# Optimization experiments

Measured on AMD Instinct MI355X. Metric: run time of the kernel, lower is better.

Reference implementation:

```python
import jax, jax.numpy as jnp
import numpy as np

DIM = 512; HEADS = 8; DH = 64; CHUNK = 64; DHID = DH * 4; MAX_LR = 1.0; EPS = 1e-6


def rmsnorm(x, w):
    return x * jax.lax.rsqrt(jnp.mean(x * x, axis=-1, keepdims=True) + EPS) * w


def mem_forward(params, x):
    # MemoryMLP(depth=2, expansion=4) wrapped in ResidualNorm
    nw, w0, w1 = params
    h = rmsnorm(x, nw)
    y = jax.nn.gelu(h @ w0) @ w1
    return y + x


def chunk_loss(params, k, lr, v):
    pred = mem_forward(params, k)            # (CHUNK, DH)
    loss = jnp.mean((pred - v) ** 2, axis=-1)  # per-token mse, (CHUNK,)
    return (loss * lr).sum(), loss


def assoc_scan(gates, inputs, prev=None):
    # h_t = g_t * h_{t-1} + x_t along axis=1 (chunks)
    def combine(a, b):
        g1, x1 = a; g2, x2 = b
        return g1 * g2, x2 + g2 * x1
    G, X = jax.lax.associative_scan(combine, (gates, inputs), axis=1)
    if prev is None:
        return X
    return X + G * prev[:, None]


def setup_inputs() -> dict:
    key = jax.random.key(0)
    ks = jax.random.split(key, 8)
    B, N = 2, 4096
    s = 0.02
    return {
        'seq': jax.random.normal(ks[0], (B, N, DIM), jnp.float32),
        'store_norm_w': jnp.ones((DIM,), jnp.float32),
        'Wk': jax.random.normal(ks[1], (DIM, HEADS * DH), jnp.float32) * s,
        'Wv': jax.random.normal(ks[2], (DIM, HEADS * DH), jnp.float32) * s,
        'Wstep': jax.random.normal(ks[3], (DIM, HEADS), jnp.float32) * s,
        'bstep': jnp.zeros((HEADS,), jnp.float32),
        'Wmom': jax.random.normal(ks[4], (DIM, HEADS), jnp.float32) * s,
        'bmom': jnp.zeros((HEADS,), jnp.float32),
        'Wdec': jax.random.normal(ks[5], (DIM, HEADS), jnp.float32) * s,
        'bdec': jnp.zeros((HEADS,), jnp.float32),
        'mem_norm_w': jnp.ones((HEADS, DH), jnp.float32),
        'mem_w0': jax.random.normal(ks[6], (HEADS, DH, DHID), jnp.float32) * s,
        'mem_w1': jax.random.normal(ks[7], (HEADS, DHID, DH), jnp.float32) * s,
    }


def reference(seq, store_norm_w, Wk, Wv, Wstep, bstep, Wmom, bmom, Wdec, bdec, mem_norm_w, mem_w0, mem_w1):
    B, N, _ = seq.shape
    nc = N // CHUNK
    bh = B * HEADS
    x = rmsnorm(seq, store_norm_w)                        # store pre-norm, (B,N,D)
    # per-token adaptive lr: 'b n h -> (b h) n', sigmoid * max_lr
    lr = jax.nn.sigmoid(x @ Wstep + bstep) * MAX_LR       # (B,N,H)
    lr = lr.transpose(0, 2, 1).reshape(bh, nc, CHUNK)
    # chunk-pooled rep (AveragePool) -> momentum / decay gates per chunk
    pooled = x.reshape(B, nc, CHUNK, DIM).mean(axis=2)    # (B,nc,D)
    mom = jax.nn.sigmoid(pooled @ Wmom + bmom).transpose(0, 2, 1).reshape(bh, nc, 1)
    decay = jax.nn.sigmoid(pooled @ Wdec + bdec).transpose(0, 2, 1).reshape(bh, nc, 1)

    def split(t):  # (B,N,H*DH) -> (bh, nc, CHUNK, DH)
        return t.reshape(B, N, HEADS, DH).transpose(0, 2, 1, 3).reshape(bh, nc, CHUNK, DH)
    k = split(x @ Wk)
    v = split(x @ Wv)

    # initial fast weights per (b h) stream: repeat 'h ... -> (b h) ...'
    params0 = (jnp.tile(mem_norm_w, (B, 1)),
               jnp.tile(mem_w0, (B, 1, 1)),
               jnp.tile(mem_w1, (B, 1, 1)))

    # per-chunk per-stream grads via vmap(grad) (all chunks share the initial weights)
    grad_fn = jax.grad(chunk_loss, has_aux=True)
    per_chunk = jax.vmap(grad_fn, in_axes=(None, 0, 0, 0))
    per_bh = jax.vmap(per_chunk, in_axes=(0, 0, 0, 0))
    grads, _ = per_bh(params0, k, lr, v)                  # tuple of (bh, nc, *shape)

    finals = []
    for g, w0 in zip(grads, params0):
        surprise = -g
        extra = (1,) * (g.ndim - 2)
        m = mom.reshape(bh, nc, *extra)
        d = decay.reshape(bh, nc, *extra)
        update = assoc_scan(m, surprise)                  # momentum scan, zero init
        wts = assoc_scan(1.0 - d, update, prev=w0)        # decay recurrence from init weights
        finals.append(wts[:, -1].reshape(bh, -1))
    return jnp.concatenate(finals, axis=-1)              # (bh, DH + DH*DHID + DHID*DH)
```

## Files before the change

### kernel.cpp

```cpp
#include <hip/hip_runtime.h>
#include <math.h>

typedef __attribute__((ext_vector_type(8)))  __bf16 bf16x8;
typedef __attribute__((ext_vector_type(4)))  float  f32x4;
typedef __attribute__((ext_vector_type(4)))  unsigned short ushort4v;
typedef __attribute__((ext_vector_type(8)))  unsigned short ushort8v;

#define MFMA16(acc, a, b) acc = __builtin_amdgcn_mfma_f32_16x16x32_bf16((a),(b),(acc),0,0,0)

__device__ inline unsigned short f2b(float f) {
    union { float f; unsigned int u; } v; v.f = f;
    unsigned int r = v.u + 0x7FFFu + ((v.u >> 16) & 1u);
    return (unsigned short)(r >> 16);
}
__device__ inline float b2f(unsigned short h) {
    union { unsigned int u; float f; } v; v.u = ((unsigned int)h) << 16;
    return v.f;
}
__device__ inline float tanh_fast(float z) {
    float e = __expf(2.0f * z);
    return 1.0f - 2.0f / (e + 1.0f);
}
__device__ inline float gelu_g(float x) {
    const float c0 = 0.7978845608028654f, c1 = 0.044715f;
    float z = c0 * x * (1.0f + c1 * x * x);
    return 0.5f * x * (1.0f + tanh_fast(z));
}
__device__ inline void gelu_both(float x, float& g, float& gp) {
    const float c0 = 0.7978845608028654f, c1 = 0.044715f;
    float x2 = x * x;
    float z  = c0 * x * (1.0f + c1 * x2);
    float t  = tanh_fast(z);
    g  = 0.5f * x * (1.0f + t);
    float dz = c0 * (1.0f + 3.0f * c1 * x2);
    gp = 0.5f * (1.0f + t) + 0.5f * x * (1.0f - t * t) * dz;
}
__device__ inline float sigmoidf(float x) { return 1.0f / (1.0f + __expf(-x)); }

__global__ __launch_bounds__(256) void k_wprep(
    const float* __restrict__ Wk, const float* __restrict__ Wv,
    const float* __restrict__ w0_g, const float* __restrict__ w1_g,
    const float* __restrict__ nw_g,
    unsigned short* __restrict__ WkvT, unsigned short* __restrict__ w0fT,
    unsigned short* __restrict__ w1T, unsigned short* __restrict__ w0N,
    unsigned short* __restrict__ w1N)
{
    const int bid = blockIdx.x, tid = threadIdx.x;
    __shared__ float tile[64][65];
    if (bid < 128) {
        int kt = bid >> 4, nt = bid & 15;
        const float* src = (nt < 8) ? Wk : Wv;
        int ncol0 = (nt & 7) * 64;
        for (int ii = 0; ii < 16; ++ii) {
            int idx = tid + ii * 256; int r = idx >> 6, cc = idx & 63;
            tile[r][cc] = src[(size_t)(kt * 64 + r) * 512 + ncol0 + cc];
        }
        __syncthreads();
        for (int ii = 0; ii < 16; ++ii) {
            int idx = tid + ii * 256; int r = idx >> 6, cc = idx & 63;
            WkvT[(size_t)(nt * 64 + r) * 512 + kt * 64 + cc] = f2b(tile[cc][r]);
        }
    } else if (bid < 160) {
        int q = bid - 128; int hh = q >> 2, it = q & 3;
        const float* w0h = w0_g + hh * 16384;
        for (int ii = 0; ii < 16; ++ii) {
            int idx = tid + ii * 256; int r = idx >> 6, cc = idx & 63;
            tile[r][cc] = w0h[r * 256 + it * 64 + cc];
        }
        __syncthreads();
        for (int ii = 0; ii < 16; ++ii) {
            int idx = tid + ii * 256; int r = idx >> 6, cc = idx & 63;
            w0fT[hh * 16384 + (it * 64 + r) * 64 + cc] = f2b(nw_g[hh * 64 + cc] * tile[cc][r]);
        }
    } else if (bid < 192) {
        int q = bid - 160; int hh = q >> 2, it = q & 3;
        const float* w1h = w1_g + hh * 16384;
        for (int ii = 0; ii < 16; ++ii) {
            int idx = tid + ii * 256; int r = idx >> 6, cc = idx & 63;
            tile[r][cc] = w1h[(it * 64 + r) * 64 + cc];
        }
        __syncthreads();
        for (int ii = 0; ii < 16; ++ii) {
            int idx = tid + ii * 256; int r = idx >> 6, cc = idx & 63;
            w1T[hh * 16384 + r * 256 + it * 64 + cc] = f2b(tile[cc][r]);
        }
    } else {
        int q = bid - 192;
        int gid = q * 2048 + tid * 8;
        const float* s; unsigned short* d;
        if (gid < 131072) { s = w0_g + gid; d = w0N + gid; }
        else              { s = w1_g + (gid - 131072); d = w1N + (gid - 131072); }
        #pragma unroll
        for (int jj = 0; jj < 8; ++jj) d[jj] = f2b(s[jj]);
    }
}

__global__ __launch_bounds__(256) void k_rms_lr(
    const float* __restrict__ seq, const float* __restrict__ wnorm,
    const float* __restrict__ Wstep, const float* __restrict__ bstep,
    unsigned short* __restrict__ xb, float* __restrict__ lrb)
{
    const int wid = threadIdx.x >> 6, lane = threadIdx.x & 63;
    const int t = blockIdx.x * 4 + wid;
    const float* row = seq + (size_t)t * 512 + lane * 8;
    float v[8];
    *(f32x4*)&v[0] = *(const f32x4*)row;
    *(f32x4*)&v[4] = *(const f32x4*)(row + 4);
    float ss = 0.f;
    #pragma unroll
    for (int j = 0; j < 8; ++j) ss += v[j] * v[j];
    #pragma unroll
    for (int o = 1; o < 64; o <<= 1) ss += __shfl_xor(ss, o);
    float rr = rsqrtf(ss * (1.0f / 512.0f) + 1e-6f);
    const float* wn = wnorm + lane * 8;
    ushort8v xs;
    float acc[8] = {0.f,0.f,0.f,0.f,0.f,0.f,0.f,0.f};
    #pragma unroll
    for (int j = 0; j < 8; ++j) {
        float xf = v[j] * rr * wn[j];
        xs[j] = f2b(xf);
        const float* wrow = Wstep + (size_t)(lane * 8 + j) * 8;
        #pragma unroll
        for (int h = 0; h < 8; ++h) acc[h] = fmaf(xf, wrow[h], acc[h]);
    }
    *(ushort8v*)(xb + (size_t)t * 512 + lane * 8) = xs;
    #pragma unroll
    for (int h = 0; h < 8; ++h) {
        #pragma unroll
        for (int o = 1; o < 64; o <<= 1) acc[h] += __shfl_xor(acc[h], o);
    }
    if (lane == 0) {
        #pragma unroll
        for (int h = 0; h < 8; ++h) lrb[(size_t)t * 8 + h] = sigmoidf(acc[h] + bstep[h]);
    }
}

__global__ __launch_bounds__(256) void k_pool(
    const unsigned short* __restrict__ xb, float* __restrict__ pooled)
{
    const int bc = blockIdx.x, tid = threadIdx.x;
    float p0 = 0.f, p1 = 0.f;
    for (int t = 0; t < 64; ++t) {
        const unsigned short* r = xb + (size_t)(bc * 64 + t) * 512;
        p0 += b2f(r[tid]); p1 += b2f(r[tid + 256]);
    }
    pooled[(size_t)bc * 512 + tid]       = p0 * (1.0f / 64.0f);
    pooled[(size_t)bc * 512 + tid + 256] = p1 * (1.0f / 64.0f);
}

__global__ __launch_bounds__(256) void k_proj(
    const unsigned short* __restrict__ xb, const unsigned short* __restrict__ WkvT,
    float* __restrict__ kb, unsigned short* __restrict__ vb)
{
    __shared__ __attribute__((aligned(16))) unsigned short As[128][72];
    __shared__ __attribute__((aligned(16))) unsigned short Bs[128][72];
    const int tid = threadIdx.x;
    const int bm = blockIdx.x >> 3, bn = blockIdx.x & 7;
    const int m0 = bm * 128, n0 = bn * 128;
    const int wid = tid >> 6, lane = tid & 63, lg = lane >> 4, lo = lane & 15;
    const int wm = wid >> 1, wn = wid & 1;
    f32x4 acc[4][4];
    #pragma unroll
    for (int i = 0; i < 4; ++i)
        #pragma unroll
        for (int j = 0; j < 4; ++j) acc[i][j] = (f32x4)0.f;

    for (int k0 = 0; k0 < 512; k0 += 64) {
        #pragma unroll
        for (int ii = 0; ii < 4; ++ii) {
            int e0 = tid * 32 + ii * 8;
            int r = e0 >> 6, c = e0 & 63;
            *(bf16x8*)&As[r][c] = *(const bf16x8*)(xb   + (size_t)(m0 + r) * 512 + k0 + c);
            *(bf16x8*)&Bs[r][c] = *(const bf16x8*)(WkvT + (size_t)(n0 + r) * 512 + k0 + c);
        }
        __syncthreads();
        #pragma unroll
        for (int ks = 0; ks < 2; ++ks) {
            bf16x8 aF[4], bF[4];
            #pragma unroll
            for (int mt = 0; mt < 4; ++mt) aF[mt] = *(const bf16x8*)&As[wm * 64 + mt * 16 + lo][ks * 32 + 8 * lg];
            #pragma unroll
            for (int nt = 0; nt < 4; ++nt) bF[nt] = *(const bf16x8*)&Bs[wn * 64 + nt * 16 + lo][ks * 32 + 8 * lg];
            #pragma unroll
            for (int mt = 0; mt < 4; ++mt)
                #pragma unroll
                for (int nt = 0; nt < 4; ++nt) MFMA16(acc[mt][nt], aF[mt], bF[nt]);
        }
        __syncthreads();
    }
    #pragma unroll
    for (int mt = 0; mt < 4; ++mt)
        #pragma unroll
        for (int nt = 0; nt < 4; ++nt)
            #pragma unroll
            for (int r = 0; r < 4; ++r) {
                int row = m0 + wm * 64 + mt * 16 + lg * 4 + r;
                int col = n0 + wn * 64 + nt * 16 + lo;
                float val = acc[mt][nt][r];
                if (col < 512) kb[(size_t)row * 512 + col] = val;
                else           vb[(size_t)row * 512 + col - 512] = f2b(val);
            }
}

__global__ __launch_bounds__(64) void k_gates(
    const float* __restrict__ pooled,
    const float* __restrict__ Wmom, const float* __restrict__ bmom,
    const float* __restrict__ Wdec, const float* __restrict__ bdec,
    float* __restrict__ momout, float* __restrict__ decout)
{
    const int bc = blockIdx.x;
    const int tid = threadIdx.x, h = tid & 7, d0 = tid >> 3;
    const float* pr = pooled + (size_t)bc * 512;
    float pm = 0.f, pd = 0.f;
    #pragma unroll 8
    for (int it = 0; it < 64; ++it) {
        int d = d0 + it * 8; float pv = pr[d];
        pm = fmaf(pv, Wmom[d * 8 + h], pm);
        pd = fmaf(pv, Wdec[d * 8 + h], pd);
    }
    #pragma unroll
    for (int o = 8; o < 64; o <<= 1) { pm += __shfl_xor(pm, o); pd += __shfl_xor(pd, o); }
    if (tid < 8) {
        momout[(size_t)bc * 8 + h] = sigmoidf(pm + bmom[h]);
        decout[(size_t)bc * 8 + h] = sigmoidf(pd + bdec[h]);
    }
}

__global__ void k_coeff(const float* __restrict__ mom, const float* __restrict__ dec,
                        float* __restrict__ coeff, float* __restrict__ Aout)
{
    int s = threadIdx.x;
    if (s >= 16) return;
    int b = s >> 3, h = s & 7;
    float P = 1.f, S = 1.f;
    coeff[s * 64 + 63] = 1.f;
    for (int cc = 62; cc >= 0; --cc) {
        float Dn = 1.f - dec[(size_t)(b * 64 + cc + 1) * 8 + h];
        float Mn = mom[(size_t)(b * 64 + cc + 1) * 8 + h];
        P *= Dn;
        S = P + Mn * S;
        coeff[s * 64 + cc] = S;
    }
    float D0 = 1.f - dec[(size_t)(b * 64) * 8 + h];
    Aout[s] = P * D0;
}

__global__ __launch_bounds__(256) void k_fwd(
    const float* __restrict__ kb, const unsigned short* __restrict__ vb,
    const float* __restrict__ lrb, const float* __restrict__ cfb,
    const unsigned short* __restrict__ w0fT, const unsigned short* __restrict__ w1T,
    unsigned short* __restrict__ uws, unsigned short* __restrict__ ews)
{
    __shared__ __attribute__((aligned(16))) unsigned short sU[64][72];
    __shared__ __attribute__((aligned(16))) unsigned short sG[64][72];
    const int tid = threadIdx.x, blk = blockIdx.x;
    const int s = blk >> 6, c = blk & 63;
    const int b = s >> 3, h = s & 7;
    const int row0 = b * 4096 + c * 64;
    const int wid = tid >> 6, lane = tid & 63, lg = lane >> 4, lo = lane & 15;
    const size_t ubase = (size_t)blk * 4096;

    for (int tt = 0; tt < 16; ++tt) {
        int t = wid * 16 + tt;
        float kv = kb[(size_t)(row0 + t) * 512 + h * 64 + lane];
        float ss = kv * kv;
        #pragma unroll
        for (int o = 1; o < 64; o <<= 1) ss += __shfl_xor(ss, o);
        float rr = rsqrtf(ss * (1.0f / 64.0f) + 1e-6f);
        sU[t][lane] = f2b(kv * rr);
    }
    __syncthreads();
    {
        int r = tid >> 2, c0 = (tid & 3) * 16;
        *(ushort8v*)(uws + ubase + r * 64 + c0)     = *(const ushort8v*)&sU[r][c0];
        *(ushort8v*)(uws + ubase + r * 64 + c0 + 8) = *(const ushort8v*)&sU[r][c0 + 8];
    }

    const unsigned short* w0h = w0fT + h * 16384;
    const unsigned short* w1h = w1T  + h * 16384;
    bf16x8 aF0 = *(const bf16x8*)&sU[wid * 16 + lo][8 * lg];
    bf16x8 aF1 = *(const bf16x8*)&sU[wid * 16 + lo][32 + 8 * lg];

    f32x4 yac[4];
    #pragma unroll
    for (int nt = 0; nt < 4; ++nt) yac[nt] = (f32x4)0.f;

    for (int is = 0; is < 4; ++is) {
        f32x4 a1[4];
        #pragma unroll
        for (int nt = 0; nt < 4; ++nt) a1[nt] = (f32x4)0.f;
        #pragma unroll
        for (int nt = 0; nt < 4; ++nt) {
            bf16x8 b0 = *(const bf16x8*)(w0h + (size_t)(is * 64 + nt * 16 + lo) * 64 + 8 * lg);
            bf16x8 b1 = *(const bf16x8*)(w0h + (size_t)(is * 64 + nt * 16 + lo) * 64 + 32 + 8 * lg);
            MFMA16(a1[nt], aF0, b0);
            MFMA16(a1[nt], aF1, b1);
        }
        if (is > 0) __syncthreads();
        #pragma unroll
        for (int nt = 0; nt < 4; ++nt)
            #pragma unroll
            for (int r = 0; r < 4; ++r) {
                int t = wid * 16 + lg * 4 + r;
                sG[t][nt * 16 + lo] = f2b(gelu_g(a1[nt][r]));
            }
        __syncthreads();
        #pragma unroll
        for (int ks = 0; ks < 2; ++ks) {
            bf16x8 aW = *(const bf16x8*)(w1h + (size_t)(wid * 16 + lo) * 256 + is * 64 + ks * 32 + 8 * lg);
            #pragma unroll
            for (int nt = 0; nt < 4; ++nt) {
                bf16x8 bG = *(const bf16x8*)&sG[nt * 16 + lo][ks * 32 + 8 * lg];
                MFMA16(yac[nt], aW, bG);
            }
        }
    }

    float coefv = cfb[s * 64 + c];
    #pragma unroll
    for (int nt = 0; nt < 4; ++nt) {
        int t = nt * 16 + lo; int grow = row0 + t;
        float sc = -coefv * lrb[(size_t)grow * 8 + h] * (2.0f / 64.0f);
        ushort4v ev;
        #pragma unroll
        for (int r = 0; r < 4; ++r) {
            int j = wid * 16 + lg * 4 + r;
            float kv = kb[(size_t)grow * 512 + h * 64 + j];
            float vv = b2f(vb[(size_t)grow * 512 + h * 64 + j]);
            ev[r] = f2b(sc * (yac[nt][r] + kv - vv));
        }
        *(ushort4v*)(ews + ubase + t * 64 + wid * 16 + lg * 4) = ev;
    }
}

__global__ __launch_bounds__(256) void k_bwd(
    const unsigned short* __restrict__ uws, const unsigned short* __restrict__ ews,
    const unsigned short* __restrict__ w0fT, const unsigned short* __restrict__ w0N,
    const unsigned short* __restrict__ w1N, const float* __restrict__ nw_g,
    float* __restrict__ pws)
{
    __shared__ __attribute__((aligned(16))) unsigned short sUt[64][72];
    __shared__ __attribute__((aligned(16))) unsigned short sUT[64][72];
    __shared__ __attribute__((aligned(16))) unsigned short sET[64][72];
    __shared__ __attribute__((aligned(16))) unsigned short sGT[64][72];
    __shared__ __attribute__((aligned(16))) unsigned short sDAT[64][72];
    __shared__ __attribute__((aligned(16))) unsigned short sDAN[64][72];
    const int tid = threadIdx.x, blk = blockIdx.x;
    const int s = blk >> 5, ksl = (blk >> 2) & 7, is = blk & 3;
    const int h = s & 7;
    const int wid = tid >> 6, lane = tid & 63, lg = lane >> 4, lo = lane & 15;

    f32x4 gw1a[4], gw0a[4];
    #pragma unroll
    for (int nt = 0; nt < 4; ++nt) { gw1a[nt] = (f32x4)0.f; gw0a[nt] = (f32x4)0.f; }
    float gnwp[4] = {0.f, 0.f, 0.f, 0.f};

    const unsigned short* w0fh = w0fT + h * 16384;
    const unsigned short* w0nh = w0N  + h * 16384;
    const unsigned short* w1nh = w1N  + h * 16384;
    const int srow = tid >> 2, sc0 = (tid & 3) * 16;

    for (int tt = 0; tt < 8; ++tt) {
        __syncthreads();
        const int chunk = ksl * 8 + tt;
        const size_t base = (size_t)(s * 64 + chunk) * 4096;
        {
            ushort8v u0 = *(const ushort8v*)(uws + base + srow * 64 + sc0);
            ushort8v u1 = *(const ushort8v*)(uws + base + srow * 64 + sc0 + 8);
            *(ushort8v*)&sUt[srow][sc0]     = u0;
            *(ushort8v*)&sUt[srow][sc0 + 8] = u1;
            #pragma unroll
            for (int jj = 0; jj < 8; ++jj) { sUT[sc0 + jj][srow] = u0[jj]; sUT[sc0 + 8 + jj][srow] = u1[jj]; }
            ushort8v e0 = *(const ushort8v*)(ews + base + srow * 64 + sc0);
            ushort8v e1 = *(const ushort8v*)(ews + base + srow * 64 + sc0 + 8);
            #pragma unroll
            for (int jj = 0; jj < 8; ++jj) { sET[sc0 + jj][srow] = e0[jj]; sET[sc0 + 8 + jj][srow] = e1[jj]; }
        }
        __syncthreads();

        f32x4 a1[4];
        #pragma unroll
        for (int nt = 0; nt < 4; ++nt) a1[nt] = (f32x4)0.f;
        bf16x8 aF0 = *(const bf16x8*)&sUt[wid * 16 + lo][8 * lg];
        bf16x8 aF1 = *(const bf16x8*)&sUt[wid * 16 + lo][32 + 8 * lg];
        #pragma unroll
        for (int nt = 0; nt < 4; ++nt) {
            bf16x8 b0 = *(const bf16x8*)(w0fh + (size_t)(is * 64 + nt * 16 + lo) * 64 + 8 * lg);
            bf16x8 b1 = *(const bf16x8*)(w0fh + (size_t)(is * 64 + nt * 16 + lo) * 64 + 32 + 8 * lg);
            MFMA16(a1[nt], aF0, b0);
            MFMA16(a1[nt], aF1, b1);
        }
        float gpv[4][4];
        #pragma unroll
        for (int nt = 0; nt < 4; ++nt) {
            ushort4v gv;
            #pragma unroll
            for (int r = 0; r < 4; ++r) {
                float g, gp; gelu_both(a1[nt][r], g, gp);
                gv[r] = f2b(g); gpv[nt][r] = gp;
            }
            *(ushort4v*)&sGT[nt * 16 + lo][wid * 16 + lg * 4] = gv;
        }

        f32x4 dga[4];
        #pragma unroll
        for (int nt = 0; nt < 4; ++nt) dga[nt] = (f32x4)0.f;
        bf16x8 eF0 = *(const bf16x8*)(ews + base + (size_t)(wid * 16 + lo) * 64 + 8 * lg);
        bf16x8 eF1 = *(const bf16x8*)(ews + base + (size_t)(wid * 16 + lo) * 64 + 32 + 8 * lg);
        #pragma unroll
        for (int nt = 0; nt < 4; ++nt) {
            bf16x8 b0 = *(const bf16x8*)(w1nh + (size_t)(is * 64 + nt * 16 + lo) * 64 + 8 * lg);
            bf16x8 b1 = *(const bf16x8*)(w1nh + (size_t)(is * 64 + nt * 16 + lo) * 64 + 32 + 8 * lg);
            MFMA16(dga[nt], eF0, b0);
            MFMA16(dga[nt], eF1, b1);
        }
        #pragma unroll
        for (int nt = 0; nt < 4; ++nt) {
            ushort4v dv;
            #pragma unroll
            for (int r = 0; r < 4; ++r) dv[r] = f2b(dga[nt][r] * gpv[nt][r]);
            *(ushort4v*)&sDAT[nt * 16 + lo][wid * 16 + lg * 4] = dv;
            #pragma unroll
            for (int r = 0; r < 4; ++r) sDAN[wid * 16 + lg * 4 + r][nt * 16 + lo] = dv[r];
        }
        __syncthreads();

        #pragma unroll
        for (int ks = 0; ks < 2; ++ks) {
            bf16x8 aG = *(const bf16x8*)&sGT[wid * 16 + lo][ks * 32 + 8 * lg];
            #pragma unroll
            for (int nt = 0; nt < 4; ++nt) {
                bf16x8 bE = *(const bf16x8*)&sET[nt * 16 + lo][ks * 32 + 8 * lg];
                MFMA16(gw1a[nt], aG, bE);
            }
        }
        #pragma unroll
        for (int ks = 0; ks < 2; ++ks) {
            bf16x8 aU = *(const bf16x8*)&sUT[wid * 16 + lo][ks * 32 + 8 * lg];
            #pragma unroll
            for (int nt = 0; nt < 4; ++nt) {
                bf16x8 bD = *(const bf16x8*)&sDAT[nt * 16 + lo][ks * 32 + 8 * lg];
                MFMA16(gw0a[nt], aU, bD);
            }
        }
        f32x4 dht[4];
        #pragma unroll
        for (int nt = 0; nt < 4; ++nt) dht[nt] = (f32x4)0.f;
        #pragma unroll
        for (int ks = 0; ks < 2; ++ks) {
            bf16x8 aW0 = *(const bf16x8*)(w0nh + (size_t)(wid * 16 + lo) * 256 + is * 64 + ks * 32 + 8 * lg);
            #pragma unroll
            for (int nt = 0; nt < 4; ++nt) {
                bf16x8 bDA = *(const bf16x8*)&sDAN[nt * 16 + lo][ks * 32 + 8 * lg];
                MFMA16(dht[nt], aW0, bDA);
            }
        }
        #pragma unroll
        for (int nt = 0; nt < 4; ++nt)
            #pragma unroll
            for (int r = 0; r < 4; ++r) {
                int t = nt * 16 + lo, d = wid * 16 + lg * 4 + r;
                gnwp[r] += b2f(sUt[t][d]) * dht[nt][r];
            }
    }

    size_t pb = (size_t)blk * 8256;
    #pragma unroll
    for (int nt = 0; nt < 4; ++nt)
        #pragma unroll
        for (int r = 0; r < 4; ++r)
            pws[pb + (size_t)(wid * 16 + lg * 4 + r) * 64 + nt * 16 + lo] = gw1a[nt][r];
    #pragma unroll
    for (int r = 0; r < 4; ++r) {
        float nwv = nw_g[h * 64 + wid * 16 + lg * 4 + r];
        #pragma unroll
        for (int nt = 0; nt < 4; ++nt)
            pws[pb + 4096 + (size_t)(wid * 16 + lg * 4 + r) * 64 + nt * 16 + lo] = nwv * gw0a[nt][r];
    }
    #pragma unroll
    for (int r = 0; r < 4; ++r) {
        #pragma unroll
        for (int o = 1; o < 16; o <<= 1) gnwp[r] += __shfl_xor(gnwp[r], o);
    }
    if (lo == 0) {
        #pragma unroll
        for (int r = 0; r < 4; ++r)
            pws[pb + 8192 + wid * 16 + lg * 4 + r] = gnwp[r];
    }
}

__global__ __launch_bounds__(256) void k_reduce(
    const float* __restrict__ pws, const float* __restrict__ Ab,
    const float* __restrict__ nw_g, const float* __restrict__ w0_g,
    const float* __restrict__ w1_g, float* __restrict__ out)
{
    int gid = blockIdx.x * 256 + threadIdx.x;
    if (gid >= 16 * 32832) return;
    int s = gid / 32832, r = gid % 32832;
    int h = s & 7;
    float A = Ab[s];
    float val;
    if (r < 64) {
        val = A * nw_g[h * 64 + r];
        #pragma unroll
        for (int ks = 0; ks < 8; ++ks)
            #pragma unroll
            for (int i2 = 0; i2 < 4; ++i2)
                val += pws[(size_t)(s * 32 + ks * 4 + i2) * 8256 + 8192 + r];
    } else if (r < 16448) {
        int rr = r - 64; int d = rr >> 8; int i = rr & 255; int i2 = i >> 6, iloc = i & 63;
        val = A * w0_g[h * 16384 + rr];
        #pragma unroll
        for (int ks = 0; ks < 8; ++ks)
            val += pws[(size_t)(s * 32 + ks * 4 + i2) * 8256 + 4096 + d * 64 + iloc];
    } else {
        int rr = r - 16448; int i = rr >> 6; int j = rr & 63; int i2 = i >> 6, iloc = i & 63;
        val = A * w1_g[h * 16384 + rr];
        #pragma unroll
        for (int ks = 0; ks < 8; ++ks)
            val += pws[(size_t)(s * 32 + ks * 4 + i2) * 8256 + iloc * 64 + j];
    }
    out[gid] = val;
}

extern "C" void kernel_launch(void* const* d_in, const int* in_sizes, int n_in,
                              void* d_out, int out_size, void* d_ws, size_t ws_size,
                              hipStream_t stream) {
    (void)in_sizes; (void)n_in; (void)out_size; (void)ws_size;
    const float* seq   = (const float*)d_in[0];
    const float* snw   = (const float*)d_in[1];
    const float* Wk    = (const float*)d_in[2];
    const float* Wv    = (const float*)d_in[3];
    const float* Wstep = (const float*)d_in[4];
    const float* bstep = (const float*)d_in[5];
    const float* Wmom  = (const float*)d_in[6];
    const float* bmom  = (const float*)d_in[7];
    const float* Wdec  = (const float*)d_in[8];
    const float* bdec  = (const float*)d_in[9];
    const float* nw_g  = (const float*)d_in[10];
    const float* w0_g  = (const float*)d_in[11];
    const float* w1_g  = (const float*)d_in[12];
    float* out = (float*)d_out;

    char* ws = (char*)d_ws;
    unsigned short* xb   = (unsigned short*)(ws + 0);
    unsigned short* WkvT = (unsigned short*)(ws + 8388608);
    float*          kb   = (float*)        (ws + 9437184);
    unsigned short* vb   = (unsigned short*)(ws + 26214400);
    unsigned short* ews  = (unsigned short*)(ws + 34603008);
    unsigned short* w0fT = (unsigned short*)(ws + 42991616);
    unsigned short* w1T  = (unsigned short*)(ws + 43253760);
    unsigned short* w0N  = (unsigned short*)(ws + 43515904);
    unsigned short* w1N  = (unsigned short*)(ws + 43778048);
    float* lrb  = (float*)(ws + 44040192);
    float* plb  = (float*)(ws + 44302336);
    float* momb = (float*)(ws + 44564480);
    float* decb = (float*)(ws + 44568576);
    float* cfb  = (float*)(ws + 44572672);
    float* Ab   = (float*)(ws + 44576768);
    unsigned short* uws = (unsigned short*)(ws + 0);
    float* pws  = (float*)(ws + 9437184);

    k_wprep <<<320, 256, 0, stream>>>(Wk, Wv, w0_g, w1_g, nw_g, WkvT, w0fT, w1T, w0N, w1N);
    k_rms_lr<<<2048, 256, 0, stream>>>(seq, snw, Wstep, bstep, xb, lrb);
    k_pool  <<<128, 256, 0, stream>>>(xb, plb);
    k_proj  <<<512, 256, 0, stream>>>(xb, WkvT, kb, vb);
    k_gates <<<128, 64, 0, stream>>>(plb, Wmom, bmom, Wdec, bdec, momb, decb);
    k_coeff <<<1, 64, 0, stream>>>(momb, decb, cfb, Ab);
    k_fwd   <<<1024, 256, 0, stream>>>(kb, vb, lrb, cfb, w0fT, w1T, uws, ews);
    k_bwd   <<<512, 256, 0, stream>>>(uws, ews, w0fT, w0N, w1N, nw_g, pws);
    k_reduce<<<2052, 256, 0, stream>>>(pws, Ab, nw_g, w0_g, w1_g, out);
}
```

Measured before the change: 146.9 us.

## Store k in bf16, precompute transposed error tile, drop LDS staging in backward

The projection now writes k as bf16 instead of fp32, which halves that intermediate's traffic. The forward kernel vector-loads k/v and also emits a transposed copy of the error tile via LDS. The backward kernel reads u, its transpose and the error operands directly from global memory instead of staging and transposing them in shared memory, which removes a sync and lowers LDS use. k_pool gets vectorized loads across four waves, and the norm-gradient partials move to a separate buffer. Rounding k to bf16 slightly changes the RMS-norm input precision, and the uncoalesced gathered reads of u in the backward kernel may cost bandwidth.

```diff
diff --git a/kernel.cpp b/kernel.cpp
--- a/kernel.cpp
+++ b/kernel.cpp
@@ -138,19 +138,30 @@
 __global__ __launch_bounds__(256) void k_pool(
     const unsigned short* __restrict__ xb, float* __restrict__ pooled)
 {
+    __shared__ float sP[4][512];
     const int bc = blockIdx.x, tid = threadIdx.x;
-    float p0 = 0.f, p1 = 0.f;
-    for (int t = 0; t < 64; ++t) {
-        const unsigned short* r = xb + (size_t)(bc * 64 + t) * 512;
-        p0 += b2f(r[tid]); p1 += b2f(r[tid + 256]);
-    }
-    pooled[(size_t)bc * 512 + tid]       = p0 * (1.0f / 64.0f);
-    pooled[(size_t)bc * 512 + tid + 256] = p1 * (1.0f / 64.0f);
+    const int q = tid >> 6, lane = tid & 63, d0 = lane * 8;
+    float p[8] = {0.f,0.f,0.f,0.f,0.f,0.f,0.f,0.f};
+    for (int tt = 0; tt < 16; ++tt) {
+        int t = q * 16 + tt;
+        ushort8v v = *(const ushort8v*)(xb + (size_t)(bc * 64 + t) * 512 + d0);
+        #pragma unroll
+        for (int j = 0; j < 8; ++j) p[j] += b2f(v[j]);
+    }
+    #pragma unroll
+    for (int j = 0; j < 8; ++j) sP[q][d0 + j] = p[j];
+    __syncthreads();
+    #pragma unroll
+    for (int half = 0; half < 2; ++half) {
+        int d = tid + half * 256;
+        pooled[(size_t)bc * 512 + d] =
+            (sP[0][d] + sP[1][d] + sP[2][d] + sP[3][d]) * (1.0f / 64.0f);
+    }
 }
 
 __global__ __launch_bounds__(256) void k_proj(
     const unsigned short* __restrict__ xb, const unsigned short* __restrict__ WkvT,
-    float* __restrict__ kb, unsigned short* __restrict__ vb)
+    unsigned short* __restrict__ kbh, unsigned short* __restrict__ vb)
 {
     __shared__ __attribute__((aligned(16))) unsigned short As[128][72];
     __shared__ __attribute__((aligned(16))) unsigned short Bs[128][72];
@@ -196,9 +207,9 @@
             for (int r = 0; r < 4; ++r) {
                 int row = m0 + wm * 64 + mt * 16 + lg * 4 + r;
                 int col = n0 + wn * 64 + nt * 16 + lo;
-                float val = acc[mt][nt][r];
-                if (col < 512) kb[(size_t)row * 512 + col] = val;
-                else           vb[(size_t)row * 512 + col - 512] = f2b(val);
+                unsigned short val = f2b(acc[mt][nt][r]);
+                if (col < 512) kbh[(size_t)row * 512 + col] = val;
+                else           vb[(size_t)row * 512 + col - 512] = val;
             }
 }
 
@@ -246,10 +257,11 @@
 }
 
 __global__ __launch_bounds__(256) void k_fwd(
-    const float* __restrict__ kb, const unsigned short* __restrict__ vb,
+    const unsigned short* __restrict__ kbh, const unsigned short* __restrict__ vb,
     const float* __restrict__ lrb, const float* __restrict__ cfb,
     const unsigned short* __restrict__ w0fT, const unsigned short* __restrict__ w1T,
-    unsigned short* __restrict__ uws, unsigned short* __restrict__ ews)
+    unsigned short* __restrict__ uws, unsigned short* __restrict__ ews,
+    unsigned short* __restrict__ ewsT)
 {
     __shared__ __attribute__((aligned(16))) unsigned short sU[64][72];
     __shared__ __attribute__((aligned(16))) unsigned short sG[64][72];
@@ -262,7 +274,7 @@
 
     for (int tt = 0; tt < 16; ++tt) {
         int t = wid * 16 + tt;
-        float kv = kb[(size_t)(row0 + t) * 512 + h * 64 + lane];
+        float kv = b2f(kbh[(size_t)(row0 + t) * 512 + h * 64 + lane]);
         float ss = kv * kv;
         #pragma unroll
         for (int o = 1; o < 64; o <<= 1) ss += __shfl_xor(ss, o);
@@ -317,34 +329,48 @@
     }
 
     float coefv = cfb[s * 64 + c];
+    ushort4v evs[4];
     #pragma unroll
     for (int nt = 0; nt < 4; ++nt) {
         int t = nt * 16 + lo; int grow = row0 + t;
         float sc = -coefv * lrb[(size_t)grow * 8 + h] * (2.0f / 64.0f);
+        ushort4v k4 = *(const ushort4v*)(kbh + (size_t)grow * 512 + h * 64 + wid * 16 + lg * 4);
+        ushort4v v4 = *(const ushort4v*)(vb  + (size_t)grow * 512 + h * 64 + wid * 16 + lg * 4);
         ushort4v ev;
         #pragma unroll
-        for (int r = 0; r < 4; ++r) {
-            int j = wid * 16 + lg * 4 + r;
-            float kv = kb[(size_t)grow * 512 + h * 64 + j];
-            float vv = b2f(vb[(size_t)grow * 512 + h * 64 + j]);
-            ev[r] = f2b(sc * (yac[nt][r] + kv - vv));
-        }
+        for (int r = 0; r < 4; ++r)
+            ev[r] = f2b(sc * (yac[nt][r] + b2f(k4[r]) - b2f(v4[r])));
+        evs[nt] = ev;
         *(ushort4v*)(ews + ubase + t * 64 + wid * 16 + lg * 4) = ev;
+    }
+
+    __syncthreads();
+    #pragma unroll
+    for (int nt = 0; nt < 4; ++nt)
+        *(ushort4v*)&sG[nt * 16 + lo][wid * 16 + lg * 4] = evs[nt];
+    __syncthreads();
+    {
+        int r2 = tid >> 2, c2 = (tid & 3) * 16;
+        ushort8v o0, o1;
+        #pragma unroll
+        for (int jj = 0; jj < 8; ++jj) o0[jj] = sG[c2 + jj][r2];
+        #pragma unroll
+        for (int jj = 0; jj < 8; ++jj) o1[jj] = sG[c2 + 8 + jj][r2];
+        *(ushort8v*)(ewsT + ubase + r2 * 64 + c2)     = o0;
+        *(ushort8v*)(ewsT + ubase + r2 * 64 + c2 + 8) = o1;
     }
 }
 
 __global__ __launch_bounds__(256) void k_bwd(
     const unsigned short* __restrict__ uws, const unsigned short* __restrict__ ews,
+    const unsigned short* __restrict__ ewsT,
     const unsigned short* __restrict__ w0fT, const unsigned short* __restrict__ w0N,
     const unsigned short* __restrict__ w1N, const float* __restrict__ nw_g,
-    float* __restrict__ pws)
-{
-    __shared__ __attribute__((aligned(16))) unsigned short sUt[64][72];
-    __shared__ __attribute__((aligned(16))) unsigned short sUT[64][72];
-    __shared__ __attribute__((aligned(16))) unsigned short sET[64][72];
+    float* __restrict__ pws, float* __restrict__ gnwb)
+{
     __shared__ __attribute__((aligned(16))) unsigned short sGT[64][72];
     __shared__ __attribute__((aligned(16))) unsigned short sDAT[64][72];
-    __shared__ __attribute__((aligned(16))) unsigned short sDAN[64][72];
+    __shared__ __attribute__((aligned(16))) unsigned short sDAN[64][68];
     const int tid = threadIdx.x, blk = blockIdx.x;
     const int s = blk >> 5, ksl = (blk >> 2) & 7, is = blk & 3;
     const int h = s & 7;
@@ -358,31 +384,24 @@
     const unsigned short* w0fh = w0fT + h * 16384;
     const unsigned short* w0nh = w0N  + h * 16384;
     const unsigned short* w1nh = w1N  + h * 16384;
-    const int srow = tid >> 2, sc0 = (tid & 3) * 16;
 
     for (int tt = 0; tt < 8; ++tt) {
         __syncthreads();
         const int chunk = ksl * 8 + tt;
         const size_t base = (size_t)(s * 64 + chunk) * 4096;
-        {
-            ushort8v u0 = *(const ushort8v*)(uws + base + srow * 64 + sc0);
-            ushort8v u1 = *(const ushort8v*)(uws + base + srow * 64 + sc0 + 8);
-            *(ushort8v*)&sUt[srow][sc0]     = u0;
-            *(ushort8v*)&sUt[srow][sc0 + 8] = u1;
-            #pragma unroll
-            for (int jj = 0; jj < 8; ++jj) { sUT[sc0 + jj][srow] = u0[jj]; sUT[sc0 + 8 + jj][srow] = u1[jj]; }
-            ushort8v e0 = *(const ushort8v*)(ews + base + srow * 64 + sc0);
-            ushort8v e1 = *(const ushort8v*)(ews + base + srow * 64 + sc0 + 8);
-            #pragma unroll
-            for (int jj = 0; jj < 8; ++jj) { sET[sc0 + jj][srow] = e0[jj]; sET[sc0 + 8 + jj][srow] = e1[jj]; }
-        }
-        __syncthreads();
+
+        unsigned short utg[16];
+        #pragma unroll
+        for (int ks = 0; ks < 2; ++ks)
+            #pragma unroll
+            for (int jj = 0; jj < 8; ++jj)
+                utg[ks * 8 + jj] = uws[base + (size_t)(ks * 32 + 8 * lg + jj) * 64 + wid * 16 + lo];
 
         f32x4 a1[4];
         #pragma unroll
         for (int nt = 0; nt < 4; ++nt) a1[nt] = (f32x4)0.f;
-        bf16x8 aF0 = *(const bf16x8*)&sUt[wid * 16 + lo][8 * lg];
-        bf16x8 aF1 = *(const bf16x8*)&sUt[wid * 16 + lo][32 + 8 * lg];
+        bf16x8 aF0 = *(const bf16x8*)(uws + base + (size_t)(wid * 16 + lo) * 64 + 8 * lg);
+        bf16x8 aF1 = *(const bf16x8*)(uws + base + (size_t)(wid * 16 + lo) * 64 + 32 + 8 * lg);
         #pragma unroll
         for (int nt = 0; nt < 4; ++nt) {
             bf16x8 b0 = *(const bf16x8*)(w0fh + (size_t)(is * 64 + nt * 16 + lo) * 64 + 8 * lg);
@@ -430,17 +449,19 @@
             bf16x8 aG = *(const bf16x8*)&sGT[wid * 16 + lo][ks * 32 + 8 * lg];
             #pragma unroll
             for (int nt = 0; nt < 4; ++nt) {
-                bf16x8 bE = *(const bf16x8*)&sET[nt * 16 + lo][ks * 32 + 8 * lg];
+                bf16x8 bE = *(const bf16x8*)(ewsT + base + (size_t)(nt * 16 + lo) * 64 + ks * 32 + 8 * lg);
                 MFMA16(gw1a[nt], aG, bE);
             }
         }
         #pragma unroll
         for (int ks = 0; ks < 2; ++ks) {
-            bf16x8 aU = *(const bf16x8*)&sUT[wid * 16 + lo][ks * 32 + 8 * lg];
+            union { ushort8v u; bf16x8 b; } cu;
+            #pragma unroll
+            for (int jj = 0; jj < 8; ++jj) cu.u[jj] = utg[ks * 8 + jj];
             #pragma unroll
             for (int nt = 0; nt < 4; ++nt) {
                 bf16x8 bD = *(const bf16x8*)&sDAT[nt * 16 + lo][ks * 32 + 8 * lg];
-                MFMA16(gw0a[nt], aU, bD);
+                MFMA16(gw0a[nt], cu.b, bD);
             }
         }
         f32x4 dht[4];
@@ -456,15 +477,15 @@
             }
         }
         #pragma unroll
-        for (int nt = 0; nt < 4; ++nt)
-            #pragma unroll
-            for (int r = 0; r < 4; ++r) {
-                int t = nt * 16 + lo, d = wid * 16 + lg * 4 + r;
-                gnwp[r] += b2f(sUt[t][d]) * dht[nt][r];
-            }
-    }
-
-    size_t pb = (size_t)blk * 8256;
+        for (int nt = 0; nt < 4; ++nt) {
+            ushort4v u4 = *(const ushort4v*)(uws + base + (size_t)(nt * 16 + lo) * 64 + wid * 16 + lg * 4);
+            #pragma unroll
+            for (int r = 0; r < 4; ++r)
+                gnwp[r] += b2f(u4[r]) * dht[nt][r];
+        }
+    }
+
+    size_t pb = (size_t)blk * 8192;
     #pragma unroll
     for (int nt = 0; nt < 4; ++nt)
         #pragma unroll
@@ -485,12 +506,13 @@
     if (lo == 0) {
         #pragma unroll
         for (int r = 0; r < 4; ++r)
-            pws[pb + 8192 + wid * 16 + lg * 4 + r] = gnwp[r];
+            gnwb[(size_t)blk * 64 + wid * 16 + lg * 4 + r] = gnwp[r];
     }
 }
 
 __global__ __launch_bounds__(256) void k_reduce(
-    const float* __restrict__ pws, const float* __restrict__ Ab,
+    const float* __restrict__ pws, const float* __restrict__ gnwb,
+    const float* __restrict__ Ab,
     const float* __restrict__ nw_g, const float* __restrict__ w0_g,
     const float* __restrict__ w1_g, float* __restrict__ out)
 {
@@ -506,19 +528,19 @@
         for (int ks = 0; ks < 8; ++ks)
             #pragma unroll
             for (int i2 = 0; i2 < 4; ++i2)
-                val += pws[(size_t)(s * 32 + ks * 4 + i2) * 8256 + 8192 + r];
+                val += gnwb[(size_t)(s * 32 + ks * 4 + i2) * 64 + r];
     } else if (r < 16448) {
         int rr = r - 64; int d = rr >> 8; int i = rr & 255; int i2 = i >> 6, iloc = i & 63;
         val = A * w0_g[h * 16384 + rr];
         #pragma unroll
         for (int ks = 0; ks < 8; ++ks)
-            val += pws[(size_t)(s * 32 + ks * 4 + i2) * 8256 + 4096 + d * 64 + iloc];
+            val += pws[(size_t)(s * 32 + ks * 4 + i2) * 8192 + 4096 + d * 64 + iloc];
     } else {
         int rr = r - 16448; int i = rr >> 6; int j = rr & 63; int i2 = i >> 6, iloc = i & 63;
         val = A * w1_g[h * 16384 + rr];
         #pragma unroll
         for (int ks = 0; ks < 8; ++ks)
-            val += pws[(size_t)(s * 32 + ks * 4 + i2) * 8256 + iloc * 64 + j];
+            val += pws[(size_t)(s * 32 + ks * 4 + i2) * 8192 + iloc * 64 + j];
     }
     out[gid] = val;
 }
@@ -544,10 +566,14 @@
 
     char* ws = (char*)d_ws;
     unsigned short* xb   = (unsigned short*)(ws + 0);
+    unsigned short* uws  = (unsigned short*)(ws + 0);
     unsigned short* WkvT = (unsigned short*)(ws + 8388608);
-    float*          kb   = (float*)        (ws + 9437184);
-    unsigned short* vb   = (unsigned short*)(ws + 26214400);
-    unsigned short* ews  = (unsigned short*)(ws + 34603008);
+    float*          gnwb = (float*)        (ws + 8388608);
+    unsigned short* kbh  = (unsigned short*)(ws + 9437184);
+    unsigned short* vb   = (unsigned short*)(ws + 17825792);
+    float*          pws  = (float*)        (ws + 9437184);
+    unsigned short* ews  = (unsigned short*)(ws + 26214400);
+    unsigned short* ewsT = (unsigned short*)(ws + 34603008);
     unsigned short* w0fT = (unsigned short*)(ws + 42991616);
     unsigned short* w1T  = (unsigned short*)(ws + 43253760);
     unsigned short* w0N  = (unsigned short*)(ws + 43515904);
@@ -558,16 +584,14 @@
     float* decb = (float*)(ws + 44568576);
     float* cfb  = (float*)(ws + 44572672);
     float* Ab   = (float*)(ws + 44576768);
-    unsigned short* uws = (unsigned short*)(ws + 0);
-    float* pws  = (float*)(ws + 9437184);
 
     k_wprep <<<320, 256, 0, stream>>>(Wk, Wv, w0_g, w1_g, nw_g, WkvT, w0fT, w1T, w0N, w1N);
     k_rms_lr<<<2048, 256, 0, stream>>>(seq, snw, Wstep, bstep, xb, lrb);
     k_pool  <<<128, 256, 0, stream>>>(xb, plb);
-    k_proj  <<<512, 256, 0, stream>>>(xb, WkvT, kb, vb);
+    k_proj  <<<512, 256, 0, stream>>>(xb, WkvT, kbh, vb);
     k_gates <<<128, 64, 0, stream>>>(plb, Wmom, bmom, Wdec, bdec, momb, decb);
     k_coeff <<<1, 64, 0, stream>>>(momb, decb, cfb, Ab);
-    k_fwd   <<<1024, 256, 0, stream>>>(kb, vb, lrb, cfb, w0fT, w1T, uws, ews);
-    k_bwd   <<<512, 256, 0, stream>>>(uws, ews, w0fT, w0N, w1N, nw_g, pws);
-    k_reduce<<<2052, 256, 0, stream>>>(pws, Ab, nw_g, w0_g, w1_g, out);
-}
+    k_fwd   <<<1024, 256, 0, stream>>>(kbh, vb, lrb, cfb, w0fT, w1T, uws, ews, ewsT);
+    k_bwd   <<<512, 256, 0, stream>>>(uws, ews, ewsT, w0fT, w0N, w1N, nw_g, pws, gnwb);
+    k_reduce<<<2052, 256, 0, stream>>>(pws, gnwb, Ab, nw_g, w0_g, w1_g, out);
+}
```

Result: slower. 152.5 us (+3.8%).
